# Performance work log

Hardware: AMD Instinct MI355X
Metric: run time of the kernel (lower is better)

Reference implementation:

```python
import jax, jax.numpy as jnp
import numpy as np

D_PROJ = 256      # core d_proj
WIN = 1536        # win_small (mid path, L<=mid_thr)
STRIDE = 384      # stride_small


def setup_inputs() -> dict:
    key = jax.random.key(0)
    ks = jax.random.split(key, 6)
    B, L, d_h, T, d_g = 4, 8192, 1024, 512, 256
    H = jax.random.normal(ks[0], (B, L, d_h), jnp.float32)
    G = jax.random.normal(ks[1], (B, T, d_g), jnp.float32)
    attn_mask = jnp.ones((B, L), dtype=bool)
    Wq_core = jax.random.normal(ks[2], (d_g, D_PROJ), jnp.float32) / np.float32(np.sqrt(d_g))
    Wk_core = jax.random.normal(ks[3], (d_h, D_PROJ), jnp.float32) / np.float32(np.sqrt(d_h))
    Wq_win = jax.random.normal(ks[4], (d_g, d_h), jnp.float32) / np.float32(np.sqrt(d_g))
    Wk_win = jax.random.normal(ks[5], (d_h, d_h), jnp.float32) / np.float32(np.sqrt(d_h))
    return dict(H=H, G=G, attn_mask=attn_mask, Wq_core=Wq_core, Wk_core=Wk_core,
                Wq_win=Wq_win, Wk_win=Wk_win)


def _core_pool(Hk, G, mask, Wq_core, Wk_core):
    # GoSpecificWattiPooling: GO-query cross-attention pooling over residues.
    q = jnp.einsum('btg,gp->btp', G, Wq_core)                 # [B,T,P]
    k = jnp.einsum('bwd,dp->bwp', Hk, Wk_core)                # [B,W,P]
    scores = jnp.einsum('btp,bwp->btw', q, k) * (D_PROJ ** -0.5)
    scores = jnp.where(mask[:, None, :], scores, jnp.float32(-1e30))
    alpha = jax.nn.softmax(scores, axis=-1)                   # over residues
    return jnp.einsum('btw,bwd->btd', alpha, Hk)              # [B,T,d_h]


def _window_starts(L, win, stride):
    starts, s = [], 0
    while s < L:
        e = min(s + win, L)
        starts.append(s)
        if e == L:
            break
        s += stride
    return starts


def reference(H, G, attn_mask, Wq_core, Wk_core, Wq_win, Wk_win):
    B, L, D = H.shape
    T = G.shape[1]
    starts = jnp.asarray(_window_starts(L, WIN, STRIDE), jnp.int32)
    q_t = jnp.einsum('btg,gd->btd', G, Wq_win)                # [B,T,D]
    scale = D ** -0.5

    def step(carry, s0):
        m, ssum, z = carry
        Hk = jax.lax.dynamic_slice_in_dim(H, s0, WIN, axis=1)
        mk = jax.lax.dynamic_slice_in_dim(attn_mask, s0, WIN, axis=1)
        Zk = _core_pool(Hk, G, mk, Wq_core, Wk_core)          # [B,T,D]
        k_w = jnp.einsum('btd,de->bte', Zk, Wk_win)
        lw = (jnp.sum(q_t * k_w, axis=-1, keepdims=True) * scale).astype(jnp.float32)
        m_new = jnp.maximum(m, lw)
        exp_m = jnp.exp(m - m_new)
        exp_w = jnp.exp(lw - m_new)
        ssum = ssum * exp_m + exp_w
        z = z * exp_m + exp_w * Zk.astype(jnp.float32)
        return (m_new, ssum, z), None

    init = (jnp.full((B, T, 1), -jnp.inf, jnp.float32),
            jnp.zeros((B, T, 1), jnp.float32),
            jnp.zeros((B, T, D), jnp.float32))
    (m, ssum, z), _ = jax.lax.scan(step, init, starts)
    return (z / (ssum + 1e-8)).astype(H.dtype)
```

## Files before the change

### kernel.cpp

```cpp
#include <hip/hip_runtime.h>
#include <math.h>

constexpr int Bb = 4;
constexpr int Lb = 8192;
constexpr int Dh = 1024;
constexpr int Tt = 512;
constexpr int Dg = 256;
constexpr int Pp = 256;
constexpr int NW = 19;

typedef unsigned short u16;
typedef __bf16 bf16x8 __attribute__((ext_vector_type(8)));
typedef float f32x4 __attribute__((ext_vector_type(4)));
typedef unsigned short us8 __attribute__((ext_vector_type(8)));

__device__ __forceinline__ u16 f2bf(float x) {
  union { float f; unsigned u; } v;
  v.f = x;
  unsigned r = v.u + 0x7FFFu + ((v.u >> 16) & 1u);
  return (u16)(r >> 16);
}
__device__ __forceinline__ float bf2f(unsigned v) {
  union { unsigned u; float f; } c;
  c.u = v << 16;
  return c.f;
}

#define GLDS16(g, l)                                                          \
  __builtin_amdgcn_global_load_lds(                                           \
      (const __attribute__((address_space(1))) void*)(g),                     \
      (__attribute__((address_space(3))) void*)(l), 16, 0, 0)

__device__ __forceinline__ void stage_A(const u16* __restrict__ A, int lda,
                                        int bm, int kA, u16* As, int tid,
                                        int wid) {
  const int rr = tid >> 3;
  const int c16 = (tid & 7) ^ (rr & 7);
#pragma unroll
  for (int cc = 0; cc < 4; cc++) {
    const int r = cc * 64 + rr;
    GLDS16(A + (long long)(bm + r) * lda + kA + c16 * 8,
           As + cc * 4096 + wid * 512);
  }
}

__device__ __forceinline__ void stage_ops(const u16* __restrict__ A, int lda,
                                          int bm, int kA, u16* As,
                                          const u16* __restrict__ B, int ldb,
                                          int bn, int kB, u16* Bs, int tid,
                                          int wid) {
  stage_A(A, lda, bm, kA, As, tid, wid);
  stage_A(B, ldb, bn, kB, Bs, tid, wid);
}

template <int OB>
__global__ __launch_bounds__(512, 1) void gemm256(const u16* __restrict__ A,
                                                  const u16* __restrict__ B,
                                                  void* __restrict__ C,
                                                  int K, int lda, int ldb,
                                                  int ldc, long long sA,
                                                  long long sB, long long sC,
                                                  long long sK, int kSplit,
                                                  float alpha) {
  __shared__ u16 lds[65536];

  const int gx = gridDim.x, gy = gridDim.y;
  int flat = blockIdx.x + gx * (blockIdx.y + gy * blockIdx.z);
  const int nwg = gx * gy * (int)gridDim.z;
  const int q = nwg >> 3, r = nwg & 7;
  const int xcd = flat & 7, sub = flat >> 3;
  flat = (xcd < r ? xcd * (q + 1) : r * (q + 1) + (xcd - r) * q) + sub;
  const int bmI = flat % gx;
  const int t1 = flat / gx;
  const int bnI = t1 % gy;
  const int z = t1 / gy;

  const int b = z / kSplit, ks = z % kSplit;
  const int kLen = K / kSplit;
  const int nt = kLen >> 6;
  A += b * sA + (long long)ks * kLen;
  B += b * sB + (long long)ks * kLen;
  const long long cOff = (long long)b * sC + (long long)ks * sK;

  const int bm = bmI * 256, bn = bnI * 256;
  const int tid = threadIdx.x;
  const int wid = tid >> 6, l = tid & 63;
  const int wm = wid >> 2, wn = wid & 3;
  const int rl = l & 15, kq = l >> 4;
  const int xr = rl & 7;

  f32x4 acc[8][4];
#pragma unroll
  for (int i = 0; i < 8; i++)
#pragma unroll
    for (int j = 0; j < 4; j++) acc[i][j] = (f32x4){0.f, 0.f, 0.f, 0.f};

  stage_ops(A, lda, bm, 0, lds, B, ldb, bn, 0, lds + 32768, tid, wid);
  stage_ops(A, lda, bm, 64, lds + 16384, B, ldb, bn, 64, lds + 49152, tid, wid);
  asm volatile("s_waitcnt vmcnt(8)" ::: "memory");
  __builtin_amdgcn_s_barrier();

  for (int t = 0; t < nt; t++) {
    const int cur = t & 1;
    const u16* As = lds + cur * 16384;
    const u16* Bs = lds + 32768 + cur * 16384;
    bf16x8 a0[4][2], bb[4][2];

#pragma unroll
    for (int i = 0; i < 4; i++)
#pragma unroll
      for (int s = 0; s < 2; s++)
        a0[i][s] = *(const bf16x8*)(As + (wm * 128 + i * 16 + rl) * 64 +
                                    (((s * 4 + kq) ^ xr) << 3));
#pragma unroll
    for (int j = 0; j < 2; j++)
#pragma unroll
      for (int s = 0; s < 2; s++)
        bb[j][s] = *(const bf16x8*)(Bs + (wn * 64 + j * 16 + rl) * 64 +
                                    (((s * 4 + kq) ^ xr) << 3));
    __builtin_amdgcn_s_barrier();
    __builtin_amdgcn_s_setprio(1);
#pragma unroll
    for (int i = 0; i < 4; i++)
#pragma unroll
      for (int j = 0; j < 2; j++)
#pragma unroll
        for (int s = 0; s < 2; s++)
          acc[i][j] = __builtin_amdgcn_mfma_f32_16x16x32_bf16(
              a0[i][s], bb[j][s], acc[i][j], 0, 0, 0);
    __builtin_amdgcn_s_setprio(0);
    __builtin_amdgcn_s_barrier();

#pragma unroll
    for (int j = 2; j < 4; j++)
#pragma unroll
      for (int s = 0; s < 2; s++)
        bb[j][s] = *(const bf16x8*)(Bs + (wn * 64 + j * 16 + rl) * 64 +
                                    (((s * 4 + kq) ^ xr) << 3));
    __builtin_amdgcn_s_barrier();
    __builtin_amdgcn_s_setprio(1);
#pragma unroll
    for (int i = 0; i < 4; i++)
#pragma unroll
      for (int j = 2; j < 4; j++)
#pragma unroll
        for (int s = 0; s < 2; s++)
          acc[i][j] = __builtin_amdgcn_mfma_f32_16x16x32_bf16(
              a0[i][s], bb[j][s], acc[i][j], 0, 0, 0);
    __builtin_amdgcn_s_setprio(0);
    __builtin_amdgcn_s_barrier();

#pragma unroll
    for (int i = 0; i < 4; i++)
#pragma unroll
      for (int s = 0; s < 2; s++)
        a0[i][s] = *(const bf16x8*)(As + (wm * 128 + 64 + i * 16 + rl) * 64 +
                                    (((s * 4 + kq) ^ xr) << 3));
    __builtin_amdgcn_s_barrier();
    __builtin_amdgcn_s_setprio(1);
#pragma unroll
    for (int i = 0; i < 4; i++)
#pragma unroll
      for (int j = 2; j < 4; j++)
#pragma unroll
        for (int s = 0; s < 2; s++)
          acc[i + 4][j] = __builtin_amdgcn_mfma_f32_16x16x32_bf16(
              a0[i][s], bb[j][s], acc[i + 4][j], 0, 0, 0);
    __builtin_amdgcn_s_setprio(0);
    __builtin_amdgcn_s_barrier();

    if (t + 2 < nt) {
      u16* Asw = (u16*)lds + cur * 16384;
      u16* Bsw = (u16*)lds + 32768 + cur * 16384;
      stage_ops(A, lda, bm, (t + 2) * 64, Asw, B, ldb, bn, (t + 2) * 64, Bsw,
                tid, wid);
    }
    __builtin_amdgcn_s_setprio(1);
#pragma unroll
    for (int i = 0; i < 4; i++)
#pragma unroll
      for (int j = 0; j < 2; j++)
#pragma unroll
        for (int s = 0; s < 2; s++)
          acc[i + 4][j] = __builtin_amdgcn_mfma_f32_16x16x32_bf16(
              a0[i][s], bb[j][s], acc[i + 4][j], 0, 0, 0);
    __builtin_amdgcn_s_setprio(0);
    if (t + 2 < nt)
      asm volatile("s_waitcnt vmcnt(8)" ::: "memory");
    else
      asm volatile("s_waitcnt vmcnt(0)" ::: "memory");
    __builtin_amdgcn_s_barrier();
  }

  float* Cf = (float*)C;
  u16* Cb = (u16*)C;
#pragma unroll
  for (int i = 0; i < 8; i++) {
    const int row0 = bm + wm * 128 + i * 16 + kq * 4;
#pragma unroll
    for (int j = 0; j < 4; j++) {
      const int col = bn + wn * 64 + j * 16 + rl;
#pragma unroll
      for (int r2 = 0; r2 < 4; r2++) {
        const float v = alpha * acc[i][j][r2];
        const long long idx = cOff + (long long)(row0 + r2) * ldc + col;
        if (OB)
          Cb[idx] = f2bf(v);
        else
          Cf[idx] = v;
      }
    }
  }
}

__global__ __launch_bounds__(512, 1) void gemm256rb(const u16* __restrict__ A,
                                                    const u16* __restrict__ B,
                                                    float* __restrict__ C,
                                                    int K, int lda, int ldb,
                                                    int ldc, long long sA,
                                                    long long sB, long long sC,
                                                    long long sK, int kSplit,
                                                    float alpha) {
  __shared__ u16 lds[65536];

  const int gx = gridDim.x, gy = gridDim.y;
  int flat = blockIdx.x + gx * (blockIdx.y + gy * blockIdx.z);
  const int nwg = gx * gy * (int)gridDim.z;
  const int q = nwg >> 3, r = nwg & 7;
  const int xcd = flat & 7, sub = flat >> 3;
  flat = (xcd < r ? xcd * (q + 1) : r * (q + 1) + (xcd - r) * q) + sub;
  const int bmI = flat % gx;
  const int t1 = flat / gx;
  const int bnI = t1 % gy;
  const int z = t1 / gy;

  const int b = z / kSplit, ks = z % kSplit;
  const int kLen = K / kSplit;
  const int nt = kLen >> 6;
  A += b * sA + (long long)ks * kLen;
  B += b * sB + (long long)ks * kLen * (long long)ldb;
  const long long cOff = (long long)b * sC + (long long)ks * sK;

  const int bm = bmI * 256, bn = bnI * 256;
  const int tid = threadIdx.x;
  const int wid = tid >> 6, l = tid & 63;
  const int wm = wid >> 2, wn = wid & 3;
  const int rl = l & 15, kq = l >> 4;
  const int xr = rl & 7;

  const int bk = tid & 63;
  const int bj = (tid >> 6) * 4;
  const int bku = bk >> 3, bkl = bk & 7;

  f32x4 acc[8][4];
#pragma unroll
  for (int i = 0; i < 8; i++)
#pragma unroll
    for (int j = 0; j < 4; j++) acc[i][j] = (f32x4){0.f, 0.f, 0.f, 0.f};

  us8 br0[4], br1[4], breg[4];
#pragma unroll
  for (int c = 0; c < 4; c++)
    br0[c] = *(const us8*)(B + (long long)(0 * 64 + bk) * ldb + bn + (bj + c) * 8);
#pragma unroll
  for (int c = 0; c < 4; c++)
    br1[c] = *(const us8*)(B + (long long)(1 * 64 + bk) * ldb + bn + (bj + c) * 8);
  stage_A(A, lda, bm, 0, lds, tid, wid);
  stage_A(A, lda, bm, 64, lds + 16384, tid, wid);
  asm volatile("s_waitcnt vmcnt(8)" ::: "memory");
  {
    u16* B0 = (u16*)lds + 32768;
    u16* B1 = (u16*)lds + 49152;
#pragma unroll
    for (int c = 0; c < 4; c++)
#pragma unroll
      for (int i = 0; i < 8; i++) {
        const int nn = 8 * (bj + c) + i;
        const int off = nn * 64 + ((bku ^ i) << 3) + bkl;
        B0[off] = br0[c][i];
        B1[off] = br1[c][i];
      }
  }
  asm volatile("s_waitcnt vmcnt(0) lgkmcnt(0)" ::: "memory");
  __builtin_amdgcn_s_barrier();

  for (int t = 0; t < nt; t++) {
    const int cur = t & 1;
    const u16* As = lds + cur * 16384;
    const u16* Bs = lds + 32768 + cur * 16384;
    bf16x8 a0[4][2], bb[4][2];

    if (t + 2 < nt) {
#pragma unroll
      for (int c = 0; c < 4; c++)
        breg[c] = *(const us8*)(B + (long long)((t + 2) * 64 + bk) * ldb + bn +
                                (bj + c) * 8);
    }
#pragma unroll
    for (int i = 0; i < 4; i++)
#pragma unroll
      for (int s = 0; s < 2; s++)
        a0[i][s] = *(const bf16x8*)(As + (wm * 128 + i * 16 + rl) * 64 +
                                    (((s * 4 + kq) ^ xr) << 3));
#pragma unroll
    for (int j = 0; j < 2; j++)
#pragma unroll
      for (int s = 0; s < 2; s++)
        bb[j][s] = *(const bf16x8*)(Bs + (wn * 64 + j * 16 + rl) * 64 +
                                    (((s * 4 + kq) ^ xr) << 3));
    __builtin_amdgcn_s_barrier();
    __builtin_amdgcn_s_setprio(1);
#pragma unroll
    for (int i = 0; i < 4; i++)
#pragma unroll
      for (int j = 0; j < 2; j++)
#pragma unroll
        for (int s = 0; s < 2; s++)
          acc[i][j] = __builtin_amdgcn_mfma_f32_16x16x32_bf16(
              a0[i][s], bb[j][s], acc[i][j], 0, 0, 0);
    __builtin_amdgcn_s_setprio(0);
    __builtin_amdgcn_s_barrier();

#pragma unroll
    for (int j = 2; j < 4; j++)
#pragma unroll
      for (int s = 0; s < 2; s++)
        bb[j][s] = *(const bf16x8*)(Bs + (wn * 64 + j * 16 + rl) * 64 +
                                    (((s * 4 + kq) ^ xr) << 3));
    __builtin_amdgcn_s_barrier();
    __builtin_amdgcn_s_setprio(1);
#pragma unroll
    for (int i = 0; i < 4; i++)
#pragma unroll
      for (int j = 2; j < 4; j++)
#pragma unroll
        for (int s = 0; s < 2; s++)
          acc[i][j] = __builtin_amdgcn_mfma_f32_16x16x32_bf16(
              a0[i][s], bb[j][s], acc[i][j], 0, 0, 0);
    __builtin_amdgcn_s_setprio(0);
    __builtin_amdgcn_s_barrier();

#pragma unroll
    for (int i = 0; i < 4; i++)
#pragma unroll
      for (int s = 0; s < 2; s++)
        a0[i][s] = *(const bf16x8*)(As + (wm * 128 + 64 + i * 16 + rl) * 64 +
                                    (((s * 4 + kq) ^ xr) << 3));
    __builtin_amdgcn_s_barrier();
    __builtin_amdgcn_s_setprio(1);
#pragma unroll
    for (int i = 0; i < 4; i++)
#pragma unroll
      for (int j = 2; j < 4; j++)
#pragma unroll
        for (int s = 0; s < 2; s++)
          acc[i + 4][j] = __builtin_amdgcn_mfma_f32_16x16x32_bf16(
              a0[i][s], bb[j][s], acc[i + 4][j], 0, 0, 0);
    __builtin_amdgcn_s_setprio(0);
    __builtin_amdgcn_s_barrier();

    if (t + 2 < nt)
      stage_A(A, lda, bm, (t + 2) * 64, (u16*)lds + cur * 16384, tid, wid);
    __builtin_amdgcn_s_setprio(1);
#pragma unroll
    for (int i = 0; i < 4; i++)
#pragma unroll
      for (int j = 0; j < 2; j++)
#pragma unroll
        for (int s = 0; s < 2; s++)
          acc[i + 4][j] = __builtin_amdgcn_mfma_f32_16x16x32_bf16(
              a0[i][s], bb[j][s], acc[i + 4][j], 0, 0, 0);
    __builtin_amdgcn_s_setprio(0);
    if (t + 2 < nt) {
      asm volatile("s_waitcnt vmcnt(4)" ::: "memory");
      u16* Bw = (u16*)lds + 32768 + cur * 16384;
#pragma unroll
      for (int c = 0; c < 4; c++)
#pragma unroll
        for (int i = 0; i < 8; i++) {
          const int nn = 8 * (bj + c) + i;
          Bw[nn * 64 + ((bku ^ i) << 3) + bkl] = breg[c][i];
        }
      asm volatile("s_waitcnt lgkmcnt(0)" ::: "memory");
    } else {
      asm volatile("s_waitcnt vmcnt(0)" ::: "memory");
    }
    __builtin_amdgcn_s_barrier();
  }

#pragma unroll
  for (int i = 0; i < 8; i++) {
    const int row0 = bm + wm * 128 + i * 16 + kq * 4;
#pragma unroll
    for (int j = 0; j < 4; j++) {
      const int col = bn + wn * 64 + j * 16 + rl;
#pragma unroll
      for (int r2 = 0; r2 < 4; r2++) {
        const long long idx = cOff + (long long)(row0 + r2) * ldc + col;
        C[idx] = alpha * acc[i][j][r2];
      }
    }
  }
}

template <int OB, int ORD>
__global__ __launch_bounds__(256) void mgemm(const u16* __restrict__ A,
                                             const u16* __restrict__ B,
                                             void* __restrict__ C,
                                             int K, int lda, int ldb, int ldc,
                                             long long sA, long long sB,
                                             long long sC, long long sK,
                                             int kSplit, float alpha) {
  __shared__ u16 smem[8192];
  u16* As = smem;
  u16* Bs = smem + 4096;

  const int gx = gridDim.x, gy = gridDim.y;
  int flat = blockIdx.x + gx * (blockIdx.y + gy * blockIdx.z);
  const int nwg = gx * gy * (int)gridDim.z;
  const int q = nwg >> 3, r = nwg & 7;
  const int xcd = flat & 7, sub = flat >> 3;
  flat = (xcd < r ? xcd * (q + 1) : r * (q + 1) + (xcd - r) * q) + sub;
  int bmI, bnI, z;
  if (ORD == 0) {
    bmI = flat % gx;
    const int t = flat / gx;
    bnI = t % gy;
    z = t / gy;
  } else {
    bnI = flat % gy;
    const int t = flat / gy;
    bmI = t % gx;
    z = t / gx;
  }

  const int b = z / kSplit, ks = z % kSplit;
  const int kLen = K / kSplit;
  A += b * sA + (long long)ks * kLen;
  B += b * sB + (long long)ks * kLen;
  const long long cOff = (long long)b * sC + (long long)ks * sK;

  const int bm = bmI * 128;
  const int bn = bnI * 128;
  const int tid = threadIdx.x;
  const int l = tid & 63;
  const int wid = tid >> 6;
  const int wm = wid >> 1, wn = wid & 1;

  const int sr = l >> 2, sj = l & 3;
  const int skb = sj ^ ((sr >> 1) & 3);

  f32x4 acc[4][4];
#pragma unroll
  for (int i = 0; i < 4; i++)
#pragma unroll
    for (int j = 0; j < 4; j++) acc[i][j] = (f32x4){0.f, 0.f, 0.f, 0.f};

  const int rl = l & 15, kb = l >> 4;

  for (int k0 = 0; k0 < kLen; k0 += 32) {
    __syncthreads();
    {
      const int c1 = wid, c2 = wid + 4;
      GLDS16(A + (long long)(bm + c1 * 16 + sr) * lda + k0 + skb * 8,
             As + c1 * 512);
      GLDS16(A + (long long)(bm + c2 * 16 + sr) * lda + k0 + skb * 8,
             As + c2 * 512);
      GLDS16(B + (long long)(bn + c1 * 16 + sr) * ldb + k0 + skb * 8,
             Bs + c1 * 512);
      GLDS16(B + (long long)(bn + c2 * 16 + sr) * ldb + k0 + skb * 8,
             Bs + c2 * 512);
    }
    __syncthreads();

    bf16x8 af[4], bfr[4];
#pragma unroll
    for (int f = 0; f < 4; f++) {
      const int rowA = wm * 64 + f * 16 + rl;
      const int unitA = rowA * 4 + (kb ^ ((rowA >> 1) & 3));
      af[f] = *(const bf16x8*)(As + unitA * 8);
      const int rowB = wn * 64 + f * 16 + rl;
      const int unitB = rowB * 4 + (kb ^ ((rowB >> 1) & 3));
      bfr[f] = *(const bf16x8*)(Bs + unitB * 8);
    }
#pragma unroll
    for (int i = 0; i < 4; i++)
#pragma unroll
      for (int j = 0; j < 4; j++)
        acc[i][j] = __builtin_amdgcn_mfma_f32_16x16x32_bf16(af[i], bfr[j],
                                                            acc[i][j], 0, 0, 0);
  }

  float* Cf = (float*)C;
  u16* Cb = (u16*)C;
#pragma unroll
  for (int i = 0; i < 4; i++) {
    const int row0 = bm + wm * 64 + i * 16 + (l >> 4) * 4;
#pragma unroll
    for (int j = 0; j < 4; j++) {
      const int col = bn + wn * 64 + j * 16 + (l & 15);
#pragma unroll
      for (int r2 = 0; r2 < 4; r2++) {
        const float v = alpha * acc[i][j][r2];
        const long long idx = cOff + (long long)(row0 + r2) * ldc + col;
        if (OB)
          Cb[idx] = f2bf(v);
        else
          Cf[idx] = v;
      }
    }
  }
}

__global__ __launch_bounds__(256) void convk(const float* __restrict__ in,
                                             u16* __restrict__ out, long long n4) {
  for (long long i = (long long)blockIdx.x * 256 + threadIdx.x; i < n4;
       i += (long long)gridDim.x * 256) {
    const float4 v = ((const float4*)in)[i];
    ushort4 o;
    o.x = f2bf(v.x);
    o.y = f2bf(v.y);
    o.z = f2bf(v.z);
    o.w = f2bf(v.w);
    ((ushort4*)out)[i] = o;
  }
}

__global__ __launch_bounds__(256) void t32(const float* __restrict__ in,
                                           u16* __restrict__ out, int R, int C,
                                           long long sIn, long long sOut) {
  __shared__ float t[32][33];
  const int b = blockIdx.z;
  in += (long long)b * sIn;
  out += (long long)b * sOut;
  const int r0 = blockIdx.x * 32, c0 = blockIdx.y * 32;
  const int tx = threadIdx.x, ty = threadIdx.y;
#pragma unroll
  for (int i = 0; i < 4; i++)
    t[ty + i * 8][tx] = in[(long long)(r0 + ty + i * 8) * C + c0 + tx];
  __syncthreads();
#pragma unroll
  for (int i = 0; i < 4; i++)
    out[(long long)(c0 + ty + i * 8) * R + r0 + tx] = f2bf(t[tx][ty + i * 8]);
}

__global__ __launch_bounds__(256) void addout8(const float* __restrict__ p,
                                               float* __restrict__ out, long long n4) {
  for (long long i = (long long)blockIdx.x * 256 + threadIdx.x; i < n4;
       i += (long long)gridDim.x * 256) {
    float4 s = ((const float4*)p)[i];
#pragma unroll
    for (int j = 1; j < 8; j++) {
      const float4 v = ((const float4*)p)[i + (long long)j * n4];
      s.x += v.x;
      s.y += v.y;
      s.z += v.z;
      s.w += v.w;
    }
    ((float4*)out)[i] = s;
  }
}

__global__ __launch_bounds__(256) void combine2(const u16* __restrict__ S,
                                                const u16* __restrict__ V,
                                                u16* __restrict__ Gm) {
  __shared__ u16 Ss[Lb];
  __shared__ float mx_s[64], se_s[64], sv_s[64], coef_s[64];
  __shared__ float m_s[NW], cw_s[NW];

  const int bt = blockIdx.x;
  const u16* Srow = S + (long long)bt * Lb;
  const u16* Vrow = V + (long long)bt * Lb;
  u16* Grow = Gm + (long long)bt * Lb;

  const int tid = threadIdx.x;
  const int ln = tid & 63;
  const int wid = tid >> 6;

  for (int i = tid; i < Lb / 8; i += 256) {
    ((uint4*)Ss)[i] = ((const uint4*)Srow)[i];
  }
  __syncthreads();

  for (int i = 0; i < 16; i++) {
    const int c = wid * 16 + i;
    const int j0 = c * 128 + ln * 2;
    const unsigned sp = *(const unsigned*)&Ss[j0];
    const float s0 = bf2f(sp & 0xffffu), s1 = bf2f(sp >> 16);
    float mx = fmaxf(s0, s1);
#pragma unroll
    for (int o = 32; o; o >>= 1) mx = fmaxf(mx, __shfl_xor(mx, o, 64));
    const unsigned vv = *(const unsigned*)(Vrow + j0);
    const float v0 = bf2f(vv & 0xffffu), v1 = bf2f(vv >> 16);
    const float e0 = __expf(s0 - mx), e1 = __expf(s1 - mx);
    float se = e0 + e1;
    float sv = e0 * v0 + e1 * v1;
#pragma unroll
    for (int o = 32; o; o >>= 1) {
      se += __shfl_xor(se, o, 64);
      sv += __shfl_xor(sv, o, 64);
    }
    if (ln == 0) {
      mx_s[c] = mx;
      se_s[c] = se;
      sv_s[c] = sv;
    }
  }
  __syncthreads();

  if (wid == 0) {
    float lw = -1e30f, mw = 0.f, dw = 1.f;
    if (ln < NW) {
      const int c0 = (ln == 18) ? 52 : 3 * ln;
      mw = -1e30f;
#pragma unroll
      for (int k = 0; k < 12; k++) mw = fmaxf(mw, mx_s[c0 + k]);
      float d = 0.f, n = 0.f;
#pragma unroll
      for (int k = 0; k < 12; k++) {
        const float r = __expf(mx_s[c0 + k] - mw);
        d = fmaf(se_s[c0 + k], r, d);
        n = fmaf(sv_s[c0 + k], r, n);
      }
      dw = d;
      lw = (n / d) * 0.03125f;
    }
    float M = lw;
#pragma unroll
    for (int o = 32; o; o >>= 1) M = fmaxf(M, __shfl_xor(M, o, 64));
    const float e = (ln < NW) ? __expf(lw - M) : 0.f;
    float ss = e;
#pragma unroll
    for (int o = 32; o; o >>= 1) ss += __shfl_xor(ss, o, 64);
    if (ln < NW) {
      m_s[ln] = mw;
      cw_s[ln] = e / (ss + 1e-8f) / dw;
    }
  }
  __syncthreads();

  if (tid < 64) {
    const int c = tid;
    const int wlo = (c <= 11) ? 0 : (c - 9) / 3;
    const int whi = min(17, c / 3);
    const float mx = mx_s[c];
    float cf = 0.f;
    for (int w = wlo; w <= whi; w++) cf = fmaf(cw_s[w], __expf(mx - m_s[w]), cf);
    if (c >= 52) cf = fmaf(cw_s[18], __expf(mx - m_s[18]), cf);
    coef_s[c] = cf;
  }
  __syncthreads();

  for (int i = tid; i < Lb / 8; i += 256) {
    const int l0 = i * 8;
    const int c = l0 >> 7;
    const float mx = mx_s[c], cf = coef_s[c];
    const us8 sp = *(const us8*)&Ss[l0];
    us8 o;
#pragma unroll
    for (int j = 0; j < 8; j++)
      o[j] = f2bf(__expf(bf2f((unsigned)sp[j]) - mx) * cf);
    *(us8*)(Grow + l0) = o;
  }
}

extern "C" void kernel_launch(void* const* d_in, const int* in_sizes, int n_in,
                              void* d_out, int out_size, void* d_ws, size_t ws_size,
                              hipStream_t stream) {
  const float* H = (const float*)d_in[0];
  const float* G = (const float*)d_in[1];
  const float* Wq_core = (const float*)d_in[3];
  const float* Wk_core = (const float*)d_in[4];
  const float* Wq_win = (const float*)d_in[5];
  const float* Wk_win = (const float*)d_in[6];
  float* out = (float*)d_out;

  const size_t MB = (size_t)1 << 20;
  char* w = (char*)d_ws;
  u16* Hb    = (u16*)(w);
  u16* gb    = (u16*)(w + 64 * MB);
  u16* Sb    = (u16*)(w + 128 * MB);
  float* part = (float*)(w + 128 * MB);
  u16* Kfb   = (u16*)(w + 192 * MB);
  u16* Vb    = (u16*)(w + 192 * MB);
  u16* qb    = (u16*)(w + 208 * MB);
  u16* qtb   = (u16*)(w + 209 * MB);
  u16* Wkwb  = (u16*)(w + 213 * MB);
  u16* WkcTb = (u16*)(w + 215 * MB);
  u16* WqcTb = (u16*)(w + 215 * MB + MB / 2);
  u16* WqwTb = (u16*)(w + 216 * MB);
  u16* Gb    = (u16*)(w + 217 * MB);
  u16* ub    = (u16*)(w + 224 * MB);

  convk<<<2048, 256, 0, stream>>>(H, Hb, (long long)Bb * Lb * Dh / 4);
  t32<<<dim3(32, 8, 1), dim3(32, 8), 0, stream>>>(Wk_core, WkcTb, Dh, Pp, 0, 0);
  t32<<<dim3(8, 8, 1), dim3(32, 8), 0, stream>>>(Wq_core, WqcTb, Dg, Pp, 0, 0);
  t32<<<dim3(8, 32, 1), dim3(32, 8), 0, stream>>>(Wq_win, WqwTb, Dg, Dh, 0, 0);
  convk<<<1024, 256, 0, stream>>>(Wk_win, Wkwb, (long long)Dh * Dh / 4);
  convk<<<512, 256, 0, stream>>>(G, Gb, (long long)Bb * Tt * Dg / 4);

  gemm256<1><<<dim3(128, 1, 1), 512, 0, stream>>>(
      Hb, WkcTb, Kfb, Dh, Dh, Dh, Pp, 0, 0, 0, 0, 1, 1.f);

  mgemm<1, 0><<<dim3(16, 2, 1), 256, 0, stream>>>(
      Gb, WqcTb, qb, Dg, Dg, Dg, Pp, 0, 0, 0, 0, 1, 1.f);

  mgemm<1, 0><<<dim3(16, 8, 1), 256, 0, stream>>>(
      Gb, WqwTb, qtb, Dg, Dg, Dg, Dh, 0, 0, 0, 0, 1, 1.f);

  mgemm<1, 0><<<dim3(16, 8, 1), 256, 0, stream>>>(
      qtb, Wkwb, ub, Dh, Dh, Dh, Dh, 0, 0, 0, 0, 1, 1.f);

  gemm256<1><<<dim3(2, 32, Bb), 512, 0, stream>>>(
      qb, Kfb, Sb, Pp, Pp, Pp, Lb, (long long)Tt * Pp, (long long)Lb * Pp,
      (long long)Tt * Lb, 0, 1, 0.0625f);

  gemm256<1><<<dim3(2, 32, Bb), 512, 0, stream>>>(
      ub, Hb, Vb, Dh, Dh, Dh, Lb, (long long)Tt * Dh, (long long)Lb * Dh,
      (long long)Tt * Lb, 0, 1, 1.f);

  combine2<<<dim3(Bb * Tt), 256, 0, stream>>>(Sb, Vb, gb);

  gemm256rb<<<dim3(2, 4, Bb * 8), 512, 0, stream>>>(
      gb, Hb, part, Lb, Lb, Dh, Dh, (long long)Tt * Lb, (long long)Lb * Dh,
      (long long)Tt * Dh, (long long)Bb * Tt * Dh, 8, 1.f);

  addout8<<<2048, 256, 0, stream>>>(part, out, (long long)Bb * Tt * Dh / 4);
}
```

Baseline: 281.9 us.

## Fold Wk_core into query side and merge score/value GEMMs into one

Instead of projecting H by Wk_core to get K and then multiplying q by K, the code first forms q·Wk_coreᵀ (a T×Dh matrix) and applies it directly to H. That removes the separate H-projection GEMM and its intermediate buffer. The score rows and the value-logit rows (u = q_t·Wk_winᵀ) are stacked into one 1024-row operand per batch, so a single gemm256 launch against H produces both S and V. Each pass now does more K-dimension work (Dh instead of Pp), but H is read once for both outputs and one launch plus one intermediate disappear.

```diff
diff --git a/kernel.cpp b/kernel.cpp
--- a/kernel.cpp
+++ b/kernel.cpp
@@ -561,16 +561,16 @@
   }
 }
 
-__global__ __launch_bounds__(256) void combine2(const u16* __restrict__ S,
-                                                const u16* __restrict__ V,
+__global__ __launch_bounds__(256) void combine2(const u16* __restrict__ SV,
                                                 u16* __restrict__ Gm) {
   __shared__ u16 Ss[Lb];
   __shared__ float mx_s[64], se_s[64], sv_s[64], coef_s[64];
   __shared__ float m_s[NW], cw_s[NW];
 
   const int bt = blockIdx.x;
-  const u16* Srow = S + (long long)bt * Lb;
-  const u16* Vrow = V + (long long)bt * Lb;
+  const int b = bt >> 9, t = bt & 511;
+  const u16* Srow = SV + ((long long)b * 1024 + t) * Lb;
+  const u16* Vrow = SV + ((long long)b * 1024 + 512 + t) * Lb;
   u16* Grow = Gm + (long long)bt * Lb;
 
   const int tid = threadIdx.x;
@@ -679,47 +679,43 @@
   char* w = (char*)d_ws;
   u16* Hb    = (u16*)(w);
   u16* gb    = (u16*)(w + 64 * MB);
-  u16* Sb    = (u16*)(w + 128 * MB);
+  u16* Asv   = (u16*)(w + 96 * MB);
+  u16* SVb   = (u16*)(w + 128 * MB);
   float* part = (float*)(w + 128 * MB);
-  u16* Kfb   = (u16*)(w + 192 * MB);
-  u16* Vb    = (u16*)(w + 192 * MB);
-  u16* qb    = (u16*)(w + 208 * MB);
-  u16* qtb   = (u16*)(w + 209 * MB);
-  u16* Wkwb  = (u16*)(w + 213 * MB);
-  u16* WkcTb = (u16*)(w + 215 * MB);
-  u16* WqcTb = (u16*)(w + 215 * MB + MB / 2);
-  u16* WqwTb = (u16*)(w + 216 * MB);
-  u16* Gb    = (u16*)(w + 217 * MB);
-  u16* ub    = (u16*)(w + 224 * MB);
+  u16* qb    = (u16*)(w + 192 * MB);
+  u16* qtb   = (u16*)(w + 193 * MB);
+  u16* Wkwb  = (u16*)(w + 197 * MB);
+  u16* Wkcb  = (u16*)(w + 199 * MB);
+  u16* WqcTb = (u16*)(w + 199 * MB + MB / 2);
+  u16* WqwTb = (u16*)(w + 200 * MB);
+  u16* Gb    = (u16*)(w + 201 * MB);
 
   convk<<<2048, 256, 0, stream>>>(H, Hb, (long long)Bb * Lb * Dh / 4);
-  t32<<<dim3(32, 8, 1), dim3(32, 8), 0, stream>>>(Wk_core, WkcTb, Dh, Pp, 0, 0);
+  convk<<<256, 256, 0, stream>>>(Wk_core, Wkcb, (long long)Dh * Pp / 4);
   t32<<<dim3(8, 8, 1), dim3(32, 8), 0, stream>>>(Wq_core, WqcTb, Dg, Pp, 0, 0);
   t32<<<dim3(8, 32, 1), dim3(32, 8), 0, stream>>>(Wq_win, WqwTb, Dg, Dh, 0, 0);
   convk<<<1024, 256, 0, stream>>>(Wk_win, Wkwb, (long long)Dh * Dh / 4);
   convk<<<512, 256, 0, stream>>>(G, Gb, (long long)Bb * Tt * Dg / 4);
 
-  gemm256<1><<<dim3(128, 1, 1), 512, 0, stream>>>(
-      Hb, WkcTb, Kfb, Dh, Dh, Dh, Pp, 0, 0, 0, 0, 1, 1.f);
-
   mgemm<1, 0><<<dim3(16, 2, 1), 256, 0, stream>>>(
       Gb, WqcTb, qb, Dg, Dg, Dg, Pp, 0, 0, 0, 0, 1, 1.f);
 
   mgemm<1, 0><<<dim3(16, 8, 1), 256, 0, stream>>>(
       Gb, WqwTb, qtb, Dg, Dg, Dg, Dh, 0, 0, 0, 0, 1, 1.f);
 
-  mgemm<1, 0><<<dim3(16, 8, 1), 256, 0, stream>>>(
-      qtb, Wkwb, ub, Dh, Dh, Dh, Dh, 0, 0, 0, 0, 1, 1.f);
-
-  gemm256<1><<<dim3(2, 32, Bb), 512, 0, stream>>>(
-      qb, Kfb, Sb, Pp, Pp, Pp, Lb, (long long)Tt * Pp, (long long)Lb * Pp,
-      (long long)Tt * Lb, 0, 1, 0.0625f);
-
-  gemm256<1><<<dim3(2, 32, Bb), 512, 0, stream>>>(
-      ub, Hb, Vb, Dh, Dh, Dh, Lb, (long long)Tt * Dh, (long long)Lb * Dh,
-      (long long)Tt * Lb, 0, 1, 1.f);
-
-  combine2<<<dim3(Bb * Tt), 256, 0, stream>>>(Sb, Vb, gb);
+  mgemm<1, 0><<<dim3(4, 8, Bb), 256, 0, stream>>>(
+      qb, Wkcb, Asv, Pp, Pp, Pp, Dh, (long long)Tt * Pp, 0,
+      (long long)1024 * Dh, 0, 1, 0.0625f);
+
+  mgemm<1, 0><<<dim3(4, 8, Bb), 256, 0, stream>>>(
+      qtb, Wkwb, Asv + (long long)512 * Dh, Dh, Dh, Dh, Dh,
+      (long long)Tt * Dh, 0, (long long)1024 * Dh, 0, 1, 1.f);
+
+  gemm256<1><<<dim3(4, 32, Bb), 512, 0, stream>>>(
+      Asv, Hb, SVb, Dh, Dh, Dh, Lb, (long long)1024 * Dh,
+      (long long)Lb * Dh, (long long)1024 * Lb, 0, 1, 1.f);
+
+  combine2<<<dim3(Bb * Tt), 256, 0, stream>>>(SVb, gb);
 
   gemm256rb<<<dim3(2, 4, Bb * 8), 512, 0, stream>>>(
       gb, Hb, part, Lb, Lb, Dh, Dh, (long long)Tt * Lb, (long long)Lb * Dh,
```

Result: faster. 270.2 us, median of 2 (-4.2%).
